# Performance work log

Hardware: AMD Instinct MI355X
Metric: run time of the kernel (lower is better)

## Reference

```python
import jax, jax.numpy as jnp
import numpy as np
from jax import lax

B, V_ECC, V_ERR, T, C = 8192, 16, 12, 25, 32
F_IN = C * T           # 800 = temporal_out * tf_num
G = 64                 # gcn_out
H2 = 256               # hidden_size * 2
EHR_DIM, EHR_OUT = 64, 64

def _lhat(V):
    # bidirectional ring graph; PyG ChebConv sym-norm with lambda_max=2.0:
    # L_hat = (2/lmax) * (I - D^-1/2 A D^-1/2) - I = -D^-1/2 A D^-1/2
    i = np.arange(V)
    src = np.concatenate([i, (i + 1) % V])
    dst = np.concatenate([(i + 1) % V, i])
    A = np.zeros((V, V), np.float32)
    A[src, dst] = 1.0
    deg = A.sum(1)
    dinv = np.where(deg > 0, deg ** -0.5, 0.0).astype(np.float32)
    return jnp.asarray(-(dinv[:, None] * A * dinv[None, :]))

LHAT_ECC = _lhat(V_ECC)
LHAT_ERR = _lhat(V_ERR)

def setup_inputs():
    key = jax.random.key(0)
    ks = jax.random.split(key, 23)
    n = lambda k, s: jax.random.normal(k, s, jnp.float32) * 0.02
    return {
        "ecc": jax.random.normal(ks[0], (B, V_ECC, T), jnp.float32),
        "err": jax.random.normal(ks[1], (B, V_ERR, T), jnp.float32),
        "ehr": jax.random.normal(ks[2], (B, EHR_DIM), jnp.float32),
        "wt_ecc": n(ks[3], (C, 1, 3)), "bt_ecc": n(ks[4], (C,)),
        "wt_err": n(ks[5], (C, 1, 3)), "bt_err": n(ks[6], (C,)),
        "W0_ecc": n(ks[7], (F_IN, G)), "W1_ecc": n(ks[8], (F_IN, G)), "b_ecc": n(ks[9], (G,)),
        "W0_err": n(ks[10], (F_IN, G)), "W1_err": n(ks[11], (F_IN, G)), "b_err": n(ks[12], (G,)),
        "Wp_ecc": n(ks[13], (V_ECC * G, H2)), "bp_ecc": n(ks[14], (H2,)),
        "Wp_err": n(ks[15], (V_ERR * G, H2)), "bp_err": n(ks[16], (H2,)),
        "Wa": n(ks[17], (H2, 1)), "ba": n(ks[18], (1,)),
        "We": n(ks[19], (EHR_DIM, EHR_OUT)), "be": n(ks[20], (EHR_OUT,)),
        "Wf2": n(ks[21], (H2 + EHR_OUT, 1)), "bf2": n(ks[22], (1,)),
    }

def _temporal(x, w, b):
    # x: [B, V, T]; Conv1d(1 -> C, k=3, padding=1) per node, then flatten (C, T)
    bb, v, t = x.shape
    y = lax.conv_general_dilated(x.reshape(bb * v, 1, t), w, (1,), "SAME",
                                 dimension_numbers=("NCH", "OIH", "NCH"))
    y = y + b[None, :, None]
    return y.reshape(bb, v, -1)        # [B, V, C*T]

def _cheb(x, lhat, w0, w1, b):
    # K=2 ChebConv: out = T0(x)@W0 + T1(x)@W1 + b, T1 = L_hat x (batched over B)
    tx1 = jnp.einsum("uv,bvd->bud", lhat, x)
    return x @ w0 + tx1 @ w1 + b

def reference(ecc, err, ehr, wt_ecc, bt_ecc, wt_err, bt_err,
              W0_ecc, W1_ecc, b_ecc, W0_err, W1_err, b_err,
              Wp_ecc, bp_ecc, Wp_err, bp_err, Wa, ba, We, be, Wf2, bf2):
    bsz = ecc.shape[0]
    ecc_f = _temporal(ecc, wt_ecc, bt_ecc)                    # [B,16,800]
    err_f = _temporal(err, wt_err, bt_err)                    # [B,12,800]
    ecc_out = _cheb(ecc_f, LHAT_ECC, W0_ecc, W1_ecc, b_ecc)   # [B,16,64]
    err_out = _cheb(err_f, LHAT_ERR, W0_err, W1_err, b_err)   # [B,12,64]
    ecc_g = ecc_out.reshape(bsz, -1) @ Wp_ecc + bp_ecc        # [B,256]
    err_g = err_out.reshape(bsz, -1) @ Wp_err + bp_err        # [B,256]
    attn = jax.nn.sigmoid(jnp.tanh(ecc_g + err_g) @ Wa + ba)  # [B,1]
    fused = attn * ecc_g + (1.0 - attn) * err_g
    ehr_p = jax.nn.relu(ehr @ We + be)                        # dropout = identity (eval)
    combined = jnp.concatenate([fused, ehr_p], axis=1)        # [B,320]
    x = jax.nn.relu(combined)
    return jax.nn.sigmoid(x @ Wf2 + bf2)                      # [B,1]
```

## Files before the change

### kernel.cpp

```cpp
#include <hip/hip_runtime.h>
#include <math.h>

#define B_TOT 8192
#define KE 400
#define KR 300
#define MEP 416
#define MRP 320

#define ROWS 16

#define SXE_LD 424
#define SXR_LD 328
#define SEH_LD 72

#define OFF_WEFF0E 0
#define OFF_WEFF1E 1600
#define OFF_WEFF0R 3200
#define OFF_WEFF1R 4800
#define OFF_CVE    6400
#define OFF_CVR    6464
#define OFF_BE     6528
#define OFF_BR     6784
#define U_AET 14080
#define U_ART (U_AET + 256 * MEP)
#define U_WET (U_ART + 256 * MRP)

typedef __attribute__((ext_vector_type(8))) short short8;
typedef __attribute__((ext_vector_type(4))) float floatx4;

__device__ __forceinline__ float sigmoidf_(float x) { return 1.f / (1.f + __expf(-x)); }
__device__ __forceinline__ float tanhf_(float x) { float e = __expf(2.f * x); return (e - 1.f) / (e + 1.f); }
__device__ __forceinline__ unsigned short f2bf(float x) {
    unsigned u = __float_as_uint(x);
    u += 0x7fffu + ((u >> 16) & 1u);
    return (unsigned short)(u >> 16);
}

__global__ __launch_bounds__(256) void fold_temporal(
    const float* __restrict__ wt_ecc, const float* __restrict__ bt_ecc,
    const float* __restrict__ wt_err, const float* __restrict__ bt_err,
    const float* __restrict__ W0_ecc, const float* __restrict__ W1_ecc, const float* __restrict__ b_ecc,
    const float* __restrict__ W0_err, const float* __restrict__ W1_err, const float* __restrict__ b_err,
    float* __restrict__ ws)
{
    const int blk = blockIdx.x;
    const int tid = threadIdx.x;
    const int cq = tid >> 6;
    const int g  = tid & 63;

    __shared__ float red[4][64];

    if (blk < 100) {
        const int m = blk / 25;
        const int tin = blk % 25;
        const bool is_err = (m >= 2);
        const float* wt = is_err ? wt_err : wt_ecc;
        const float* W = (m & 1) ? (is_err ? W1_err : W1_ecc) : (is_err ? W0_err : W0_ecc);
        const int t0 = tin > 0 ? tin - 1 : 0;
        const int t1 = tin < 24 ? tin + 1 : 24;
        float s = 0.f;
        #pragma unroll
        for (int c8 = 0; c8 < 8; ++c8) {
            const int c = cq * 8 + c8;
            for (int t = t0; t <= t1; ++t) {
                const int k = tin - t + 1;
                s = fmaf(wt[c * 3 + k], W[(c * 25 + t) * 64 + g], s);
            }
        }
        red[cq][g] = s;
        __syncthreads();
        if (tid < 64)
            ws[m * 1600 + tin * 64 + g] = red[0][g] + red[1][g] + red[2][g] + red[3][g];
    } else if (blk < 102) {
        const bool is_err = (blk == 101);
        const float* bt = is_err ? bt_err : bt_ecc;
        const float* W0 = is_err ? W0_err : W0_ecc;
        const float* W1 = is_err ? W1_err : W1_ecc;
        const float* bb = is_err ? b_err : b_ecc;
        float s = 0.f;
        #pragma unroll
        for (int c8 = 0; c8 < 8; ++c8) {
            const int c = cq * 8 + c8;
            const float btc = bt[c];
            #pragma unroll
            for (int t = 0; t < 25; ++t) {
                const int ct = (c * 25 + t) * 64 + g;
                s = fmaf(btc, W0[ct] - W1[ct], s);
            }
        }
        red[cq][g] = s;
        __syncthreads();
        if (tid < 64)
            ws[(is_err ? OFF_CVR : OFF_CVE) + g] =
                bb[g] + red[0][g] + red[1][g] + red[2][g] + red[3][g];
    } else {
        ws[OFF_BE + tid] = 0.f;
        ws[OFF_BR + tid] = 0.f;
    }
}

__global__ __launch_bounds__(256) void fold_graph(
    const float* __restrict__ Wp_ecc, const float* __restrict__ bp_ecc,
    const float* __restrict__ Wp_err, const float* __restrict__ bp_err,
    const float* __restrict__ We,
    float* __restrict__ wsf, unsigned short* __restrict__ wsu)
{
    const int blk = blockIdx.x;
    const int h = threadIdx.x;

    if (blk < MEP) {
        const int k = blk;
        float s = 0.f;
        if (k < KE) {
            const int v = k / 25, tin = k % 25;
            const int vp = (v + 1) & 15, vm = (v + 15) & 15;
            const float* w0 = wsf + OFF_WEFF0E + tin * 64;
            const float* w1 = wsf + OFF_WEFF1E + tin * 64;
            #pragma unroll 4
            for (int g = 0; g < 64; ++g) {
                s = fmaf(w0[g], Wp_ecc[(v * 64 + g) * 256 + h], s);
                s = fmaf(-0.5f * w1[g], Wp_ecc[(vp * 64 + g) * 256 + h] + Wp_ecc[(vm * 64 + g) * 256 + h], s);
            }
        }
        wsu[U_AET + (size_t)h * MEP + k] = f2bf(s);
    } else if (blk < MEP + MRP) {
        const int k = blk - MEP;
        float s = 0.f;
        if (k < KR) {
            const int v = k / 25, tin = k % 25;
            const int vp = (v + 1) % 12, vm = (v + 11) % 12;
            const float* w0 = wsf + OFF_WEFF0R + tin * 64;
            const float* w1 = wsf + OFF_WEFF1R + tin * 64;
            #pragma unroll 4
            for (int g = 0; g < 64; ++g) {
                s = fmaf(w0[g], Wp_err[(v * 64 + g) * 256 + h], s);
                s = fmaf(-0.5f * w1[g], Wp_err[(vp * 64 + g) * 256 + h] + Wp_err[(vm * 64 + g) * 256 + h], s);
            }
        }
        wsu[U_ART + (size_t)h * MRP + k] = f2bf(s);
    } else if (blk < MEP + MRP + 16) {
        const int i = blk - (MEP + MRP);
        const float* cv = wsf + OFF_CVE;
        float s = (i == 0) ? bp_ecc[h] : 0.f;
        #pragma unroll 4
        for (int jj = 0; jj < 64; ++jj) {
            const int j = i * 64 + jj;
            s = fmaf(cv[j & 63], Wp_ecc[(size_t)j * 256 + h], s);
        }
        atomicAdd(&wsf[OFF_BE + h], s);
    } else if (blk < MEP + MRP + 32) {
        const int i = blk - (MEP + MRP + 16);
        const float* cv = wsf + OFF_CVR;
        float s = (i == 0) ? bp_err[h] : 0.f;
        if (i < 12) {
            #pragma unroll 4
            for (int jj = 0; jj < 64; ++jj) {
                const int j = i * 64 + jj;
                s = fmaf(cv[j & 63], Wp_err[(size_t)j * 256 + h], s);
            }
        }
        atomicAdd(&wsf[OFF_BR + h], s);
    } else {
        for (int it = 0; it < 16; ++it) {
            const int idx = it * 256 + h;
            const int e = idx >> 6, d = idx & 63;
            wsu[U_WET + e * 64 + d] = f2bf(We[d * 64 + e]);
        }
    }
}

__global__ __launch_bounds__(256, 3) void fused_main(
    const float* __restrict__ ecc, const float* __restrict__ err, const float* __restrict__ ehr,
    const float* __restrict__ wsf, const unsigned short* __restrict__ wsu,
    const float* __restrict__ Wa, const float* __restrict__ ba,
    const float* __restrict__ be_, const float* __restrict__ Wf2, const float* __restrict__ bf2,
    float* __restrict__ out)
{
    const unsigned short* awt_e = wsu + U_AET;
    const unsigned short* awt_r = wsu + U_ART;
    const unsigned short* wet   = wsu + U_WET;
    const float* biasE = wsf + OFF_BE;
    const float* biasR = wsf + OFF_BR;

    __shared__ __align__(16) char smem[ROWS * SXE_LD * 2 + ROWS * SXR_LD * 2 + ROWS * SEH_LD * 2];
    unsigned short* sxe = (unsigned short*)smem;
    unsigned short* sxr = sxe + ROWS * SXE_LD;
    unsigned short* seh = sxr + ROWS * SXR_LD;
    float* pa_part = (float*)smem;
    float* at_arr  = pa_part + 64;
    float* po_part = at_arr + 16;

    const int tid = threadIdx.x;
    const int row0 = blockIdx.x * ROWS;

    for (int it = 0; it < 7; ++it) {
        const int f = it * 256 + tid;
        if (f < ROWS * 106) {
            const int r = f / 106, q = f - r * 106;
            float4 v = make_float4(0.f, 0.f, 0.f, 0.f);
            if (q < 100) v = *(const float4*)(ecc + (size_t)(row0 + r) * KE + q * 4);
            const unsigned p0 = (unsigned)f2bf(v.x) | ((unsigned)f2bf(v.y) << 16);
            const unsigned p1 = (unsigned)f2bf(v.z) | ((unsigned)f2bf(v.w) << 16);
            *(uint2*)&sxe[r * SXE_LD + q * 4] = make_uint2(p0, p1);
        }
    }
    for (int it = 0; it < 6; ++it) {
        const int f = it * 256 + tid;
        if (f < ROWS * 82) {
            const int r = f / 82, q = f - r * 82;
            float4 v = make_float4(0.f, 0.f, 0.f, 0.f);
            if (q < 75) v = *(const float4*)(err + (size_t)(row0 + r) * KR + q * 4);
            const unsigned p0 = (unsigned)f2bf(v.x) | ((unsigned)f2bf(v.y) << 16);
            const unsigned p1 = (unsigned)f2bf(v.z) | ((unsigned)f2bf(v.w) << 16);
            *(uint2*)&sxr[r * SXR_LD + q * 4] = make_uint2(p0, p1);
        }
    }
    {
        const int r = tid >> 4, q = tid & 15;
        const float4 v = *(const float4*)(ehr + (size_t)(row0 + r) * 64 + q * 4);
        const unsigned p0 = (unsigned)f2bf(v.x) | ((unsigned)f2bf(v.y) << 16);
        const unsigned p1 = (unsigned)f2bf(v.z) | ((unsigned)f2bf(v.w) << 16);
        *(uint2*)&seh[r * SEH_LD + q * 4] = make_uint2(p0, p1);
    }
    __syncthreads();

    const int wv = tid >> 6, lane = tid & 63;
    const int lm = lane & 15, lq = lane >> 4;
    const int n0 = wv * 64;

    floatx4 accE[4], accR[4], accH;
    accH = (floatx4){0.f, 0.f, 0.f, 0.f};
    #pragma unroll
    for (int nt = 0; nt < 4; ++nt) {
        accE[nt] = (floatx4){0.f, 0.f, 0.f, 0.f};
        accR[nt] = (floatx4){0.f, 0.f, 0.f, 0.f};
    }

    #pragma unroll
    for (int kc = 0; kc < 2; ++kc) {
        const short8 b = *(const short8*)(wet + (wv * 16 + lm) * 64 + kc * 32 + lq * 8);
        const short8 a = *(const short8*)&seh[lm * SEH_LD + kc * 32 + lq * 8];
        accH = __builtin_amdgcn_mfma_f32_16x16x32_bf16(a, b, accH, 0, 0, 0);
    }
    #pragma unroll
    for (int kc = 0; kc < 13; ++kc) {
        const short8 a0 = *(const short8*)&sxe[lm * SXE_LD + kc * 32 + lq * 8];
        #pragma unroll
        for (int nt = 0; nt < 4; ++nt) {
            const short8 b = *(const short8*)(awt_e + (size_t)(n0 + nt * 16 + lm) * MEP + kc * 32 + lq * 8);
            accE[nt] = __builtin_amdgcn_mfma_f32_16x16x32_bf16(a0, b, accE[nt], 0, 0, 0);
        }
    }
    #pragma unroll
    for (int kc = 0; kc < 10; ++kc) {
        const short8 a0 = *(const short8*)&sxr[lm * SXR_LD + kc * 32 + lq * 8];
        #pragma unroll
        for (int nt = 0; nt < 4; ++nt) {
            const short8 b = *(const short8*)(awt_r + (size_t)(n0 + nt * 16 + lm) * MRP + kc * 32 + lq * 8);
            accR[nt] = __builtin_amdgcn_mfma_f32_16x16x32_bf16(a0, b, accR[nt], 0, 0, 0);
        }
    }

    float bE[4], bR[4], wa[4], wf[4];
    #pragma unroll
    for (int nt = 0; nt < 4; ++nt) {
        const int h = n0 + nt * 16 + lm;
        bE[nt] = biasE[h]; bR[nt] = biasR[h]; wa[nt] = Wa[h]; wf[nt] = Wf2[h];
    }
    const int e_lane = wv * 16 + lm;
    const float eh_be = be_[e_lane];
    const float eh_wf = Wf2[256 + e_lane];

    float pa_lane[4];
    #pragma unroll
    for (int rg = 0; rg < 4; ++rg) {
        float s = 0.f;
        #pragma unroll
        for (int nt = 0; nt < 4; ++nt) {
            const float ev = accE[nt][rg] + bE[nt];
            const float rv = accR[nt][rg] + bR[nt];
            s = fmaf(tanhf_(ev + rv), wa[nt], s);
        }
        s += __shfl_xor(s, 1, 64); s += __shfl_xor(s, 2, 64);
        s += __shfl_xor(s, 4, 64); s += __shfl_xor(s, 8, 64);
        pa_lane[rg] = s;
    }

    __syncthreads();
    if (lm == 0) {
        #pragma unroll
        for (int rg = 0; rg < 4; ++rg)
            pa_part[wv * 16 + lq * 4 + rg] = pa_lane[rg];
    }
    __syncthreads();
    if (tid < 16)
        at_arr[tid] = sigmoidf_(pa_part[tid] + pa_part[16 + tid] + pa_part[32 + tid] + pa_part[48 + tid] + ba[0]);
    __syncthreads();

    float po_lane[4];
    #pragma unroll
    for (int rg = 0; rg < 4; ++rg) {
        const int r = lq * 4 + rg;
        const float at = at_arr[r];
        const float om = 1.f - at;
        float s = 0.f;
        #pragma unroll
        for (int nt = 0; nt < 4; ++nt) {
            const float ev = accE[nt][rg] + bE[nt];
            const float rv = accR[nt][rg] + bR[nt];
            s = fmaf(fmaxf(at * ev + om * rv, 0.f), wf[nt], s);
        }
        s = fmaf(fmaxf(accH[rg] + eh_be, 0.f), eh_wf, s);
        s += __shfl_xor(s, 1, 64); s += __shfl_xor(s, 2, 64);
        s += __shfl_xor(s, 4, 64); s += __shfl_xor(s, 8, 64);
        po_lane[rg] = s;
    }
    if (lm == 0) {
        #pragma unroll
        for (int rg = 0; rg < 4; ++rg)
            po_part[wv * 16 + lq * 4 + rg] = po_lane[rg];
    }
    __syncthreads();
    if (tid < 16)
        out[row0 + tid] = sigmoidf_(po_part[tid] + po_part[16 + tid] + po_part[32 + tid] + po_part[48 + tid] + bf2[0]);
}

extern "C" void kernel_launch(void* const* d_in, const int* in_sizes, int n_in,
                              void* d_out, int out_size, void* d_ws, size_t ws_size,
                              hipStream_t stream)
{
    (void)in_sizes; (void)n_in; (void)out_size; (void)ws_size;
    const float* ecc    = (const float*)d_in[0];
    const float* err    = (const float*)d_in[1];
    const float* ehr    = (const float*)d_in[2];
    const float* wt_ecc = (const float*)d_in[3];
    const float* bt_ecc = (const float*)d_in[4];
    const float* wt_err = (const float*)d_in[5];
    const float* bt_err = (const float*)d_in[6];
    const float* W0_ecc = (const float*)d_in[7];
    const float* W1_ecc = (const float*)d_in[8];
    const float* b_ecc  = (const float*)d_in[9];
    const float* W0_err = (const float*)d_in[10];
    const float* W1_err = (const float*)d_in[11];
    const float* b_err  = (const float*)d_in[12];
    const float* Wp_ecc = (const float*)d_in[13];
    const float* bp_ecc = (const float*)d_in[14];
    const float* Wp_err = (const float*)d_in[15];
    const float* bp_err = (const float*)d_in[16];
    const float* Wa     = (const float*)d_in[17];
    const float* ba     = (const float*)d_in[18];
    const float* We     = (const float*)d_in[19];
    const float* be     = (const float*)d_in[20];
    const float* Wf2    = (const float*)d_in[21];
    const float* bf2    = (const float*)d_in[22];
    float* wsf = (float*)d_ws;
    unsigned short* wsu = (unsigned short*)d_ws;
    float* out = (float*)d_out;

    fold_temporal<<<dim3(103), dim3(256), 0, stream>>>(
        wt_ecc, bt_ecc, wt_err, bt_err, W0_ecc, W1_ecc, b_ecc, W0_err, W1_err, b_err, wsf);
    fold_graph<<<dim3(MEP + MRP + 32 + 1), dim3(256), 0, stream>>>(
        Wp_ecc, bp_ecc, Wp_err, bp_err, We, wsf, wsu);
    fused_main<<<dim3(B_TOT / ROWS), dim3(256), 0, stream>>>(
        ecc, err, ehr, wsf, wsu, Wa, ba, be, Wf2, bf2, out);
}
```

Measured before the change: 147.0 us.

## Stream B weight tiles into LDS via async global_load_lds triple buffer

The main GEMM loop used to read the folded weight matrices straight from global memory into registers. It now prefetches each k-chunk of weights per wave into a swizzled three-slot LDS ring with global_load_lds, keeping two chunks in flight and managing waits with explicit vmcnt counts. This is meant to overlap weight loads with MFMA work and reduce global-load latency stalls. The LDS footprint grows by 48KB, so launch bounds drop from 3 to 2 blocks per SM, which reduces occupancy; the hand-tuned waitcnt logic is fragile.

After: 144.8 us. No clear change (-1.5%).

```diff
diff --git a/kernel.cpp b/kernel.cpp
--- a/kernel.cpp
+++ b/kernel.cpp
@@ -12,6 +12,7 @@
 #define SXE_LD 424
 #define SXR_LD 328
 #define SEH_LD 72
+#define A_BYTES (ROWS * (SXE_LD + SXR_LD + SEH_LD) * 2)
 
 #define OFF_WEFF0E 0
 #define OFF_WEFF1E 1600
@@ -35,6 +36,11 @@
     u += 0x7fffu + ((u >> 16) & 1u);
     return (unsigned short)(u >> 16);
 }
+__device__ __forceinline__ void gload_lds16(const unsigned short* g, unsigned short* l) {
+    __builtin_amdgcn_global_load_lds(
+        (const __attribute__((address_space(1))) void*)g,
+        (__attribute__((address_space(3))) void*)l, 16, 0, 0);
+}
 
 __global__ __launch_bounds__(256) void fold_temporal(
     const float* __restrict__ wt_ecc, const float* __restrict__ bt_ecc,
@@ -169,7 +175,7 @@
     }
 }
 
-__global__ __launch_bounds__(256, 3) void fused_main(
+__global__ __launch_bounds__(256, 2) void fused_main(
     const float* __restrict__ ecc, const float* __restrict__ err, const float* __restrict__ ehr,
     const float* __restrict__ wsf, const unsigned short* __restrict__ wsu,
     const float* __restrict__ Wa, const float* __restrict__ ba,
@@ -182,16 +188,35 @@
     const float* biasE = wsf + OFF_BE;
     const float* biasR = wsf + OFF_BR;
 
-    __shared__ __align__(16) char smem[ROWS * SXE_LD * 2 + ROWS * SXR_LD * 2 + ROWS * SEH_LD * 2];
+    __shared__ __align__(16) char smem[A_BYTES + 3 * 16384];
     unsigned short* sxe = (unsigned short*)smem;
     unsigned short* sxr = sxe + ROWS * SXE_LD;
     unsigned short* seh = sxr + ROWS * SXR_LD;
+    unsigned short* bbuf = (unsigned short*)(smem + A_BYTES);
     float* pa_part = (float*)smem;
     float* at_arr  = pa_part + 64;
     float* po_part = at_arr + 16;
 
     const int tid = threadIdx.x;
     const int row0 = blockIdx.x * ROWS;
+    const int wv = tid >> 6, lane = tid & 63;
+    const int lm = lane & 15, lq = lane >> 4;
+    const int n0 = wv * 64;
+
+    const int srow = lane >> 2;
+    const int scol = ((lane & 3) ^ ((lane >> 3) & 3)) * 8;
+    const unsigned short* geb = awt_e + (size_t)(n0 + srow) * MEP + scol;
+    const unsigned short* grb = awt_r + (size_t)(n0 + srow) * MRP + scol;
+
+    {
+        unsigned short* ld0 = bbuf + 0 * 8192 + wv * 2048;
+        unsigned short* ld1 = bbuf + 1 * 8192 + wv * 2048;
+        #pragma unroll
+        for (int j = 0; j < 4; ++j) {
+            gload_lds16(geb + (size_t)j * 16 * MEP + 0 * 32, ld0 + j * 512);
+            gload_lds16(geb + (size_t)j * 16 * MEP + 1 * 32, ld1 + j * 512);
+        }
+    }
 
     for (int it = 0; it < 7; ++it) {
         const int f = it * 256 + tid;
@@ -224,10 +249,6 @@
     }
     __syncthreads();
 
-    const int wv = tid >> 6, lane = tid & 63;
-    const int lm = lane & 15, lq = lane >> 4;
-    const int n0 = wv * 64;
-
     floatx4 accE[4], accR[4], accH;
     accH = (floatx4){0.f, 0.f, 0.f, 0.f};
     #pragma unroll
@@ -242,22 +263,45 @@
         const short8 a = *(const short8*)&seh[lm * SEH_LD + kc * 32 + lq * 8];
         accH = __builtin_amdgcn_mfma_f32_16x16x32_bf16(a, b, accH, 0, 0, 0);
     }
-    #pragma unroll
-    for (int kc = 0; kc < 13; ++kc) {
-        const short8 a0 = *(const short8*)&sxe[lm * SXE_LD + kc * 32 + lq * 8];
-        #pragma unroll
-        for (int nt = 0; nt < 4; ++nt) {
-            const short8 b = *(const short8*)(awt_e + (size_t)(n0 + nt * 16 + lm) * MEP + kc * 32 + lq * 8);
-            accE[nt] = __builtin_amdgcn_mfma_f32_16x16x32_bf16(a0, b, accE[nt], 0, 0, 0);
-        }
-    }
-    #pragma unroll
-    for (int kc = 0; kc < 10; ++kc) {
-        const short8 a0 = *(const short8*)&sxr[lm * SXR_LD + kc * 32 + lq * 8];
-        #pragma unroll
-        for (int nt = 0; nt < 4; ++nt) {
-            const short8 b = *(const short8*)(awt_r + (size_t)(n0 + nt * 16 + lm) * MRP + kc * 32 + lq * 8);
-            accR[nt] = __builtin_amdgcn_mfma_f32_16x16x32_bf16(a0, b, accR[nt], 0, 0, 0);
+
+    const int rswz = (lq ^ ((lm >> 1) & 3)) * 8;
+    #pragma unroll
+    for (int kc = 0; kc < 23; ++kc) {
+        if (kc <= 20) {
+            const int c = kc + 2;
+            unsigned short* ld = bbuf + (size_t)(c % 3) * 8192 + wv * 2048;
+            if (c < 13) {
+                #pragma unroll
+                for (int j = 0; j < 4; ++j)
+                    gload_lds16(geb + (size_t)j * 16 * MEP + c * 32, ld + j * 512);
+            } else {
+                #pragma unroll
+                for (int j = 0; j < 4; ++j)
+                    gload_lds16(grb + (size_t)j * 16 * MRP + (c - 13) * 32, ld + j * 512);
+            }
+            asm volatile("s_waitcnt vmcnt(8)" ::: "memory");
+        } else if (kc == 21) {
+            asm volatile("s_waitcnt vmcnt(4)" ::: "memory");
+        } else {
+            asm volatile("s_waitcnt vmcnt(0)" ::: "memory");
+        }
+        __builtin_amdgcn_sched_barrier(0);
+
+        const unsigned short* slab = bbuf + (size_t)(kc % 3) * 8192 + wv * 2048;
+        if (kc < 13) {
+            const short8 a0 = *(const short8*)&sxe[lm * SXE_LD + kc * 32 + lq * 8];
+            #pragma unroll
+            for (int nt = 0; nt < 4; ++nt) {
+                const short8 b = *(const short8*)(slab + (nt * 16 + lm) * 32 + rswz);
+                accE[nt] = __builtin_amdgcn_mfma_f32_16x16x32_bf16(a0, b, accE[nt], 0, 0, 0);
+            }
+        } else {
+            const short8 a0 = *(const short8*)&sxr[lm * SXR_LD + (kc - 13) * 32 + lq * 8];
+            #pragma unroll
+            for (int nt = 0; nt < 4; ++nt) {
+                const short8 b = *(const short8*)(slab + (nt * 16 + lm) * 32 + rswz);
+                accR[nt] = __builtin_amdgcn_mfma_f32_16x16x32_bf16(a0, b, accR[nt], 0, 0, 0);
+            }
         }
     }
 
```
